# Kernel tuning notes

Measured on AMD Instinct MI355X. Metric: run time of the kernel, lower is better.

The kernel has to match this reference:

```python
import jax, jax.numpy as jnp
import numpy as np

NUM_HEADS = 32
NUM_KV_HEADS = 8
HEAD_DIM = 128


def setup_inputs() -> dict:
    key = jax.random.key(0)
    ks = jax.random.split(key, 5)
    B, S, H = 2, 2048, 4096
    Dq = NUM_HEADS * HEAD_DIM      # 4096
    Dkv = NUM_KV_HEADS * HEAD_DIM  # 1024
    return {
        "hidden_states": jax.random.normal(ks[0], (B, S, H), jnp.float32),
        "w_q": jax.random.normal(ks[1], (H, Dq), jnp.float32) * 0.02,
        "w_k": jax.random.normal(ks[2], (H, Dkv), jnp.float32) * 0.02,
        "w_v": jax.random.normal(ks[3], (H, Dkv), jnp.float32) * 0.02,
        "w_o": jax.random.normal(ks[4], (Dq, H), jnp.float32) * 0.02,
    }


def reference(hidden_states, w_q, w_k, w_v, w_o):
    # GQA causal attention, prefill path (no KV cache, RoPE is a no-op in source).
    B, S, _ = hidden_states.shape
    Hq, Hkv, D = NUM_HEADS, NUM_KV_HEADS, HEAD_DIM
    g = Hq // Hkv  # kv groups
    scale = D ** -0.5

    q = (hidden_states @ w_q).reshape(B, S, Hkv, g, D)  # [B,S,Hkv,g,D]
    k = (hidden_states @ w_k).reshape(B, S, Hkv, D)     # [B,S,Hkv,D]
    v = (hidden_states @ w_v).reshape(B, S, Hkv, D)

    # repeat_kv expressed as grouped einsum (avoids materializing repeated K/V)
    scores = jnp.einsum('bqhgd,bkhd->bhgqk', q, k) * scale  # [B,Hkv,g,S,S]
    causal = jnp.tril(jnp.ones((S, S), dtype=bool))
    scores = jnp.where(causal, scores, -jnp.inf)
    probs = jax.nn.softmax(scores.astype(jnp.float32), axis=-1).astype(q.dtype)

    attn = jnp.einsum('bhgqk,bkhd->bqhgd', probs, v)  # [B,S,Hkv,g,D]
    attn = attn.reshape(B, S, Hq * D)
    return attn @ w_o
```

## Files before the change

kernel.cpp:

```cpp
#include <hip/hip_runtime.h>

typedef unsigned short u16;
typedef __attribute__((ext_vector_type(8))) short bf16x8;
typedef __attribute__((ext_vector_type(8))) unsigned short u16x8;
typedef __attribute__((ext_vector_type(4))) unsigned short u16x4;
typedef __attribute__((ext_vector_type(4))) float f32x4;

__device__ __forceinline__ u16 f2bf(float f) {
  union { float f; unsigned u; } v; v.f = f;
  unsigned r = v.u + 0x7fffu + ((v.u >> 16) & 1u);
  return (u16)(r >> 16);
}

__device__ __forceinline__ void gload16(const u16* g, u16* l) {
  __builtin_amdgcn_global_load_lds((const __attribute__((address_space(1))) void*)g,
                                   (__attribute__((address_space(3))) void*)l, 16, 0, 0);
}

__global__ __launch_bounds__(256) void cast_bf16_kern(const float* __restrict__ in,
                                                      u16* __restrict__ out, int n) {
  int i = (blockIdx.x * 256 + threadIdx.x) * 8;
  if (i >= n) return;
  float4 a = *(const float4*)(in + i);
  float4 b = *(const float4*)(in + i + 4);
  u16x8 r;
  r[0] = f2bf(a.x); r[1] = f2bf(a.y); r[2] = f2bf(a.z); r[3] = f2bf(a.w);
  r[4] = f2bf(b.x); r[5] = f2bf(b.y); r[6] = f2bf(b.z); r[7] = f2bf(b.w);
  *(u16x8*)(out + i) = r;
}

__global__ __launch_bounds__(256) void transpose_cast_kern(const float* __restrict__ in,
                                                           u16* __restrict__ out, int K, int N) {
  __shared__ float tile[64][65];
  int nbx = N >> 6;
  int n0 = (blockIdx.x % nbx) << 6;
  int k0 = (blockIdx.x / nbx) << 6;
  int tx = threadIdx.x & 15;
  int ty = threadIdx.x >> 4;
#pragma unroll
  for (int r = 0; r < 64; r += 16) {
    float4 v = *(const float4*)(in + (size_t)(k0 + ty + r) * N + n0 + tx * 4);
    tile[ty + r][tx * 4 + 0] = v.x;
    tile[ty + r][tx * 4 + 1] = v.y;
    tile[ty + r][tx * 4 + 2] = v.z;
    tile[ty + r][tx * 4 + 3] = v.w;
  }
  __syncthreads();
#pragma unroll
  for (int r = 0; r < 64; r += 16) {
    u16x4 o;
#pragma unroll
    for (int j = 0; j < 4; j++) o[j] = f2bf(tile[tx * 4 + j][ty + r]);
    *(u16x4*)(out + (size_t)(n0 + ty + r) * K + k0 + tx * 4) = o;
  }
}

#define FENCE() asm volatile("" ::: "memory")
#define BARRIER() do { FENCE(); __builtin_amdgcn_s_barrier(); FENCE(); } while (0)

template <int MODE>
__global__ __launch_bounds__(256, 2) void gemm256(const u16* __restrict__ A,
                                                  const u16* __restrict__ Bt,
                                                  void* __restrict__ Cout,
                                                  int M, int N, int K) {
  __shared__ u16 lds[24576];
  const int tid = threadIdx.x;
  const int lane = tid & 63, w = tid >> 6;
  const int wm = w >> 1, wn = w & 1;
  const int li = lane & 15, lg = lane >> 4;
  const int NT = K >> 5;

  const int nbn = N >> 7;
  const int nwg = gridDim.x;
  const int swz = (blockIdx.x & 7) * (nwg >> 3) + (blockIdx.x >> 3);
  const int m0 = (swz / nbn) << 8;
  const int n0 = (swz % nbn) << 7;

  const int ssl = ((lane & 3) ^ ((lane >> 3) & 3)) * 8;
  const u16* sA = A + (size_t)(m0 + w * 64 + (lane >> 2)) * K + ssl;
  const u16* sB = Bt + (size_t)(n0 + w * 32 + (lane >> 2)) * K + ssl;
  const size_t i16K = (size_t)16 * K;
  u16* dA = lds + w * 2048;
  u16* dB = lds + 16384 + w * 1024;

#define STGA(t_) do { int db_ = (t_) & 1;                                    \
    _Pragma("unroll")                                                        \
    for (int i_ = 0; i_ < 4; i_++)                                           \
      gload16(sA + (size_t)(t_) * 32 + i_ * i16K, dA + db_ * 8192 + i_ * 512); \
  } while (0)
#define STGB(t_) do { int db_ = (t_) & 1;                                    \
    _Pragma("unroll")                                                        \
    for (int j_ = 0; j_ < 2; j_++)                                           \
      gload16(sB + (size_t)(t_) * 32 + j_ * i16K, dB + db_ * 4096 + j_ * 512); \
  } while (0)

  STGA(0); STGB(0); STGB(1);
  asm volatile("s_waitcnt vmcnt(2)" ::: "memory");
  BARRIER();

  f32x4 acc[8][4];
#pragma unroll
  for (int m = 0; m < 8; m++)
#pragma unroll
    for (int n = 0; n < 4; n++) acc[m][n] = (f32x4){0.f, 0.f, 0.f, 0.f};

  const int xsl = (lg ^ ((li >> 1) & 3)) * 8;
  const int aoff = (wm * 128 + li) * 32 + xsl;
  const int boff = 16384 + (wn * 64 + li) * 32 + xsl;

  bf16x8 a[8], b[4];

  for (int t = 0; t < NT; ++t) {
    const int db = t & 1;
    const int ao = db * 8192 + aoff;
    const int bo = db * 4096 + boff;

#pragma unroll
    for (int mf = 0; mf < 4; mf++) a[mf] = *(const bf16x8*)(lds + ao + mf * 512);
#pragma unroll
    for (int nf = 0; nf < 4; nf++) b[nf] = *(const bf16x8*)(lds + bo + nf * 512);
    if (t + 1 < NT) STGA(t + 1);
    __builtin_amdgcn_s_setprio(1);
#pragma unroll
    for (int mf = 0; mf < 4; mf++)
#pragma unroll
      for (int nf = 0; nf < 4; nf++)
        acc[mf][nf] = __builtin_amdgcn_mfma_f32_16x16x32_bf16(a[mf], b[nf], acc[mf][nf], 0, 0, 0);
    __builtin_amdgcn_s_setprio(0);
    BARRIER();

#pragma unroll
    for (int mf = 4; mf < 8; mf++) a[mf] = *(const bf16x8*)(lds + ao + mf * 512);
    if (t + 2 < NT) STGB(t + 2);
    __builtin_amdgcn_s_setprio(1);
#pragma unroll
    for (int mf = 4; mf < 8; mf++)
#pragma unroll
      for (int nf = 0; nf < 4; nf++)
        acc[mf][nf] = __builtin_amdgcn_mfma_f32_16x16x32_bf16(a[mf], b[nf], acc[mf][nf], 0, 0, 0);
    __builtin_amdgcn_s_setprio(0);
    if (t < NT - 2) {
      asm volatile("s_waitcnt vmcnt(2)" ::: "memory");
    } else {
      asm volatile("s_waitcnt vmcnt(0)" ::: "memory");
    }
    BARRIER();
  }

#pragma unroll
  for (int mf = 0; mf < 8; mf++)
#pragma unroll
    for (int nf = 0; nf < 4; nf++)
#pragma unroll
      for (int r = 0; r < 4; r++) {
        int gm = m0 + wm * 128 + mf * 16 + lg * 4 + r;
        int gn = n0 + wn * 64 + nf * 16 + li;
        if (MODE == 0)
          ((u16*)Cout)[(size_t)gm * N + gn] = f2bf(acc[mf][nf][r]);
        else
          ((float*)Cout)[(size_t)gm * N + gn] = acc[mf][nf][r];
      }
#undef STGA
#undef STGB
}

__global__ __launch_bounds__(512, 2) void gemm_kv(const u16* __restrict__ A,
                                                  const u16* __restrict__ Bt,
                                                  u16* __restrict__ Kout,
                                                  u16* __restrict__ Vout) {
  __shared__ u16 lds[49152];
  const int tid = threadIdx.x;
  const int lane = tid & 63, w = tid >> 6;
  const int wm = w >> 2, wn = w & 3;
  const int li = lane & 15, lg = lane >> 4;
  const int K = 4096, NT = 64;

  const int swz = (blockIdx.x & 7) * 32 + (blockIdx.x >> 3);
  const int m0 = (swz >> 3) << 7;
  const int n0 = (swz & 7) << 8;

  const int srow = w * 16 + (lane >> 3);
  const int scol = ((lane & 7) ^ (lane >> 3)) << 3;
  const u16* sA  = A  + (size_t)(m0 + srow) * K + scol;
  const u16* sB0 = Bt + (size_t)(n0 + srow) * K + scol;
  const u16* sB1 = Bt + (size_t)(n0 + 128 + srow) * K + scol;
  const size_t jK = (size_t)8 * K;
  u16* dA  = lds + w * 1024;
  u16* dB0 = lds + 16384 + w * 1024;
  u16* dB1 = lds + 16384 + 8192 + w * 1024;

#define STGA(t_) do { int db_ = (t_) & 1;                                     \
    gload16(sA + (size_t)(t_) * 64, dA + db_ * 8192);                         \
    gload16(sA + (size_t)(t_) * 64 + jK, dA + db_ * 8192 + 512); } while (0)
#define STGB(t_) do { int db_ = (t_) & 1;                                     \
    gload16(sB0 + (size_t)(t_) * 64, dB0 + db_ * 16384);                      \
    gload16(sB0 + (size_t)(t_) * 64 + jK, dB0 + db_ * 16384 + 512);           \
    gload16(sB1 + (size_t)(t_) * 64, dB1 + db_ * 16384);                      \
    gload16(sB1 + (size_t)(t_) * 64 + jK, dB1 + db_ * 16384 + 512); } while (0)

  STGA(0); STGB(0); STGB(1);
  asm volatile("s_waitcnt vmcnt(4)" ::: "memory");
  __builtin_amdgcn_s_barrier();
  asm volatile("" ::: "memory");

  f32x4 acc[4][4];
#pragma unroll
  for (int m = 0; m < 4; m++)
#pragma unroll
    for (int n = 0; n < 4; n++) acc[m][n] = (f32x4){0.f, 0.f, 0.f, 0.f};

  const int xsw = (li & 7) << 3;
  const int k0o = (lg * 8) ^ xsw;
  const int k1o = (32 + lg * 8) ^ xsw;
  const int arow0 = wm * 64;
  const u16* bBase0 = lds + 16384 + (wn >> 1) * 8192;
  const int brow0 = (wn & 1) * 64;

  bf16x8 a[4][2], b[4][2];

  for (int t = 0; t < NT; ++t) {
    const int db = t & 1;
    const u16* Ab = lds + db * 8192;
    const u16* Bb = bBase0 + db * 16384;

#pragma unroll
    for (int mf = 0; mf < 2; mf++) {
      int r = arow0 + mf * 16 + li;
      a[mf][0] = *(const bf16x8*)(Ab + r * 64 + k0o);
      a[mf][1] = *(const bf16x8*)(Ab + r * 64 + k1o);
    }
#pragma unroll
    for (int nf = 0; nf < 4; nf++) {
      int r = brow0 + nf * 16 + li;
      b[nf][0] = *(const bf16x8*)(Bb + r * 64 + k0o);
      b[nf][1] = *(const bf16x8*)(Bb + r * 64 + k1o);
    }
    if (t + 1 < NT) STGA(t + 1);
    BARRIER();
    __builtin_amdgcn_s_setprio(1);
#pragma unroll
    for (int mf = 0; mf < 2; mf++)
#pragma unroll
      for (int nf = 0; nf < 4; nf++) {
        acc[mf][nf] = __builtin_amdgcn_mfma_f32_16x16x32_bf16(a[mf][0], b[nf][0], acc[mf][nf], 0, 0, 0);
        acc[mf][nf] = __builtin_amdgcn_mfma_f32_16x16x32_bf16(a[mf][1], b[nf][1], acc[mf][nf], 0, 0, 0);
      }
    __builtin_amdgcn_s_setprio(0);
    BARRIER();

#pragma unroll
    for (int mf = 2; mf < 4; mf++) {
      int r = arow0 + mf * 16 + li;
      a[mf][0] = *(const bf16x8*)(Ab + r * 64 + k0o);
      a[mf][1] = *(const bf16x8*)(Ab + r * 64 + k1o);
    }
    if (t + 2 < NT) STGB(t + 2);
    BARRIER();
    __builtin_amdgcn_s_setprio(1);
#pragma unroll
    for (int mf = 2; mf < 4; mf++)
#pragma unroll
      for (int nf = 0; nf < 4; nf++) {
        acc[mf][nf] = __builtin_amdgcn_mfma_f32_16x16x32_bf16(a[mf][0], b[nf][0], acc[mf][nf], 0, 0, 0);
        acc[mf][nf] = __builtin_amdgcn_mfma_f32_16x16x32_bf16(a[mf][1], b[nf][1], acc[mf][nf], 0, 0, 0);
      }
    __builtin_amdgcn_s_setprio(0);
    if (t < NT - 2) {
      asm volatile("s_waitcnt vmcnt(4)" ::: "memory");
    } else {
      asm volatile("s_waitcnt vmcnt(0)" ::: "memory");
    }
    __builtin_amdgcn_s_barrier();
    asm volatile("" ::: "memory");
  }

#pragma unroll
  for (int mf = 0; mf < 4; mf++)
#pragma unroll
    for (int nf = 0; nf < 4; nf++)
#pragma unroll
      for (int r = 0; r < 4; r++) {
        int gm = m0 + wm * 64 + mf * 16 + lg * 4 + r;
        int gn = n0 + wn * 64 + nf * 16 + li;
        float val = acc[mf][nf][r];
        if (gn < 1024) {
          Kout[(size_t)gm * 1024 + gn] = f2bf(val);
        } else {
          int c = gn - 1024;
          int b = gm >> 11, s = gm & 2047, kvh = c >> 7, d = c & 127;
          int s2 = (s & ~31) | (((s >> 2) & 3) << 3) | (((s >> 4) & 1) << 2) | (s & 3);
          Vout[(size_t)((b * 8 + kvh) * 128 + d) * 2048 + s2] = f2bf(val);
        }
      }
#undef STGA
#undef STGB
}

__global__ __launch_bounds__(256, 2) void flash_attn_kern(const u16* __restrict__ Qg,
                                                          const u16* __restrict__ Kg,
                                                          const u16* __restrict__ VT,
                                                          u16* __restrict__ Og) {
  const int bid = blockIdx.x;
  const int qt = 63 - (bid >> 4);
  const int gh = bid & 15;
  const int b = gh >> 3, kvh = gh & 7;
  const int tid = threadIdx.x;
  const int lane = tid & 63, w = tid >> 6;
  const int li = lane & 15, lg = lane >> 4;
  const int h = kvh * 4 + w;
  const int q0 = qt << 5;
  const int nt = (qt >> 1) + 1;

  __shared__ u16 Kbuf[2][8192];
  __shared__ u16 Vbuf[2][8192];

  bf16x8 qf[2][4];
  {
    const u16* qp = Qg + ((size_t)(b * 2048 + q0 + li)) * 4096 + h * 128 + lg * 8;
#pragma unroll
    for (int m = 0; m < 2; m++)
#pragma unroll
      for (int ks = 0; ks < 4; ks++)
        qf[m][ks] = *(const bf16x8*)(qp + (size_t)(m * 16) * 4096 + ks * 32);
  }

  const u16* ksrc[4];
  const u16* vsrc[4];
#pragma unroll
  for (int i = 0; i < 4; i++) {
    int c = w * 4 + i;
    int krow = c * 4 + (lane >> 4);
    int kinner = ((lane & 15) * 16) ^ ((krow & 7) << 4);
    ksrc[i] = Kg + (size_t)(b * 2048 + krow) * 1024 + kvh * 128 + (kinner >> 1);
    int vrow = c * 8 + (lane >> 3);
    int vinner = ((lane & 7) * 16) ^ ((vrow & 7) << 4);
    vsrc[i] = VT + (size_t)((b * 8 + kvh) * 128 + vrow) * 2048 + (vinner >> 1);
  }
#pragma unroll
  for (int i = 0; i < 4; i++) {
    int c = w * 4 + i;
    gload16(ksrc[i], &Kbuf[0][c * 512]);
    gload16(vsrc[i], &Vbuf[0][c * 512]);
    ksrc[i] += 64 * 1024;
    vsrc[i] += 64;
  }

  f32x4 oa[2][8];
#pragma unroll
  for (int m = 0; m < 2; m++)
#pragma unroll
    for (int n = 0; n < 8; n++) oa[m][n] = (f32x4){0.f, 0.f, 0.f, 0.f};
  f32x4 lacc[2];
  lacc[0] = (f32x4){0.f, 0.f, 0.f, 0.f};
  lacc[1] = (f32x4){0.f, 0.f, 0.f, 0.f};
  float mrun[2] = {-1e30f, -1e30f};

  const float scale = 0.08838834764831845f;
  bf16x8 onesf;
#pragma unroll
  for (int j = 0; j < 8; j++) onesf[j] = (short)0x3F80;

  asm volatile("s_waitcnt vmcnt(0)\n\ts_barrier" ::: "memory");

  for (int t = 0; t < nt; ++t) {
    const int cur = t & 1;
    const u16* KB = Kbuf[cur];
    const u16* VB = Vbuf[cur];
    if (t + 1 < nt) {
#pragma unroll
      for (int i = 0; i < 4; i++) {
        int c = w * 4 + i;
        gload16(ksrc[i], &Kbuf[cur ^ 1][c * 512]);
        gload16(vsrc[i], &Vbuf[cur ^ 1][c * 512]);
        ksrc[i] += 64 * 1024;
        vsrc[i] += 64;
      }
    }

    f32x4 sacc[2][4];
#pragma unroll
    for (int m = 0; m < 2; m++)
#pragma unroll
      for (int n = 0; n < 4; n++) sacc[m][n] = (f32x4){0.f, 0.f, 0.f, 0.f};
    __builtin_amdgcn_s_setprio(1);
#pragma unroll
    for (int n = 0; n < 4; n++) {
      int krow = n * 16 + li;
      const u16* kb = KB + krow * 128;
      int sw = (krow & 7) << 4;
#pragma unroll
      for (int ks = 0; ks < 4; ks++) {
        bf16x8 kf = *(const bf16x8*)(kb + (((ks * 64 + lg * 16) ^ sw) >> 1));
        sacc[0][n] = __builtin_amdgcn_mfma_f32_16x16x32_bf16(kf, qf[0][ks], sacc[0][n], 0, 0, 0);
        sacc[1][n] = __builtin_amdgcn_mfma_f32_16x16x32_bf16(kf, qf[1][ks], sacc[1][n], 0, 0, 0);
      }
    }
    __builtin_amdgcn_s_setprio(0);

#pragma unroll
    for (int m = 0; m < 2; m++)
#pragma unroll
      for (int n = 0; n < 4; n++)
#pragma unroll
        for (int r = 0; r < 4; r++) sacc[m][n][r] *= scale;
    if (t == nt - 1) {
      const int kv0 = t * 64;
#pragma unroll
      for (int m = 0; m < 2; m++) {
        int q = q0 + m * 16 + li;
#pragma unroll
        for (int n = 0; n < 4; n++)
#pragma unroll
          for (int r = 0; r < 4; r++)
            if (kv0 + n * 16 + lg * 4 + r > q) sacc[m][n][r] = -1e30f;
      }
    }

#pragma unroll
    for (int m = 0; m < 2; m++) {
      float mx = sacc[m][0][0];
#pragma unroll
      for (int n = 0; n < 4; n++)
#pragma unroll
        for (int r = 0; r < 4; r++) mx = fmaxf(mx, sacc[m][n][r]);
      mx = fmaxf(mx, __shfl_xor(mx, 16, 64));
      mx = fmaxf(mx, __shfl_xor(mx, 32, 64));
      float mnew = fmaxf(mrun[m], mx);
      float corr = __expf(mrun[m] - mnew);
      mrun[m] = mnew;
#pragma unroll
      for (int n = 0; n < 4; n++)
#pragma unroll
        for (int r = 0; r < 4; r++) sacc[m][n][r] = __expf(sacc[m][n][r] - mnew);
#pragma unroll
      for (int r = 0; r < 4; r++) lacc[m][r] *= corr;
#pragma unroll
      for (int n = 0; n < 8; n++)
#pragma unroll
        for (int r = 0; r < 4; r++) oa[m][n][r] *= corr;
    }

    bf16x8 pf[2][2];
#pragma unroll
    for (int m = 0; m < 2; m++)
#pragma unroll
      for (int kvs = 0; kvs < 2; kvs++) {
        u16x8 pw;
#pragma unroll
        for (int e = 0; e < 8; e++) pw[e] = f2bf(sacc[m][2 * kvs + (e >> 2)][e & 3]);
        pf[m][kvs] = *(bf16x8*)&pw;
      }

    __builtin_amdgcn_s_setprio(1);
#pragma unroll
    for (int kvs = 0; kvs < 2; kvs++) {
#pragma unroll
      for (int n = 0; n < 8; n++) {
        int vrow = n * 16 + li;
        bf16x8 vf = *(const bf16x8*)(VB + vrow * 64 +
                                     (((kvs * 64 + lg * 16) ^ ((vrow & 7) << 4)) >> 1));
        oa[0][n] = __builtin_amdgcn_mfma_f32_16x16x32_bf16(vf, pf[0][kvs], oa[0][n], 0, 0, 0);
        oa[1][n] = __builtin_amdgcn_mfma_f32_16x16x32_bf16(vf, pf[1][kvs], oa[1][n], 0, 0, 0);
      }
      lacc[0] = __builtin_amdgcn_mfma_f32_16x16x32_bf16(onesf, pf[0][kvs], lacc[0], 0, 0, 0);
      lacc[1] = __builtin_amdgcn_mfma_f32_16x16x32_bf16(onesf, pf[1][kvs], lacc[1], 0, 0, 0);
    }
    __builtin_amdgcn_s_setprio(0);

    asm volatile("s_waitcnt vmcnt(0)\n\ts_barrier" ::: "memory");
  }

#pragma unroll
  for (int m = 0; m < 2; m++) {
    float inv = 1.0f / lacc[m][0];
    u16* op = Og + (size_t)(b * 2048 + q0 + m * 16 + li) * 4096 + h * 128 + lg * 4;
#pragma unroll
    for (int n = 0; n < 8; n++) {
      u16x4 o;
#pragma unroll
      for (int r = 0; r < 4; r++) o[r] = f2bf(oa[m][n][r] * inv);
      *(u16x4*)(op + n * 16) = o;
    }
  }
}

extern "C" void kernel_launch(void* const* d_in, const int* in_sizes, int n_in,
                              void* d_out, int out_size, void* d_ws, size_t ws_size,
                              hipStream_t stream) {
  (void)in_sizes; (void)n_in; (void)out_size; (void)ws_size;
  const float* hs = (const float*)d_in[0];
  const float* wq = (const float*)d_in[1];
  const float* wk = (const float*)d_in[2];
  const float* wv = (const float*)d_in[3];
  const float* wo = (const float*)d_in[4];

  u16* ws   = (u16*)d_ws;
  u16* hs_b = ws;
  u16* wqT  = hs_b + 16777216;
  u16* wkT  = wqT + 16777216;
  u16* wvT  = wkT + 4194304;
  u16* woT  = wvT + 4194304;
  u16* Qb   = woT + 16777216;
  u16* Kb   = Qb + 16777216;
  u16* VTb  = Kb + 4194304;
  u16* attnb = VTb + 4194304;

  cast_bf16_kern<<<8192, 256, 0, stream>>>(hs, hs_b, 16777216);
  transpose_cast_kern<<<4096, 256, 0, stream>>>(wq, wqT, 4096, 4096);
  transpose_cast_kern<<<1024, 256, 0, stream>>>(wk, wkT, 4096, 1024);
  transpose_cast_kern<<<1024, 256, 0, stream>>>(wv, wvT, 4096, 1024);
  transpose_cast_kern<<<4096, 256, 0, stream>>>(wo, woT, 4096, 4096);

  gemm256<0><<<512, 256, 0, stream>>>(hs_b, wqT, Qb, 4096, 4096, 4096);
  gemm_kv<<<256, 512, 0, stream>>>(hs_b, wkT, Kb, VTb);

  flash_attn_kern<<<1024, 256, 0, stream>>>(Qb, Kb, VTb, attnb);

  gemm256<2><<<512, 256, 0, stream>>>(attnb, woT, (float*)d_out, 4096, 4096, 4096);
}
```

Baseline: 500.7 us.

## Rewrite Q/O projection GEMM as 256x256 tile with 8-wave ping-pong pipeline

The Q and output projection GEMM moves to a 256x256 block tile with 512 threads and a 64-wide k-step. It uses four-way split A/B LDS buffers, explicit ds_read_b128 inline asm with immediate offsets, and lgkmcnt-controlled interleaving of global-to-LDS prefetch with MFMA quarters. The aim is to raise arithmetic intensity per LDS and global byte and to overlap loads with compute more finely. The 128KB LDS footprint limits occupancy to one block per CU, and the grid shrinks to 256 blocks.

```diff
diff --git a/kernel.cpp b/kernel.cpp
--- a/kernel.cpp
+++ b/kernel.cpp
@@ -16,6 +16,19 @@
   __builtin_amdgcn_global_load_lds((const __attribute__((address_space(1))) void*)g,
                                    (__attribute__((address_space(3))) void*)l, 16, 0, 0);
 }
+
+template <int OFF>
+__device__ __forceinline__ bf16x8 dsr(unsigned a) {
+  static_assert(OFF >= 0 && OFF < 65536, "ds offset");
+  bf16x8 r;
+  asm volatile("ds_read_b128 %0, %1 offset:%2" : "=&v"(r) : "v"(a), "n"(OFF));
+  return r;
+}
+
+#define FENCE() asm volatile("" ::: "memory")
+#define BARRIER() do { FENCE(); __builtin_amdgcn_s_barrier(); FENCE(); } while (0)
+#define LGKM(n) do { asm volatile("s_waitcnt lgkmcnt(" #n ")" ::: "memory"); \
+                     __builtin_amdgcn_sched_barrier(0); } while (0)
 
 __global__ __launch_bounds__(256) void cast_bf16_kern(const float* __restrict__ in,
                                                       u16* __restrict__ out, int n) {
@@ -55,47 +68,49 @@
   }
 }
 
-#define FENCE() asm volatile("" ::: "memory")
-#define BARRIER() do { FENCE(); __builtin_amdgcn_s_barrier(); FENCE(); } while (0)
-
 template <int MODE>
-__global__ __launch_bounds__(256, 2) void gemm256(const u16* __restrict__ A,
+__global__ __launch_bounds__(512, 2) void gemm256(const u16* __restrict__ A,
                                                   const u16* __restrict__ Bt,
                                                   void* __restrict__ Cout,
                                                   int M, int N, int K) {
-  __shared__ u16 lds[24576];
+  __shared__ u16 lds[65536];
   const int tid = threadIdx.x;
   const int lane = tid & 63, w = tid >> 6;
-  const int wm = w >> 1, wn = w & 1;
+  const int wm = w >> 2, wn = w & 3;
   const int li = lane & 15, lg = lane >> 4;
-  const int NT = K >> 5;
-
-  const int nbn = N >> 7;
+  const int NT = K >> 6, NU = NT >> 1;
+
+  const int nbx = N >> 8;
   const int nwg = gridDim.x;
   const int swz = (blockIdx.x & 7) * (nwg >> 3) + (blockIdx.x >> 3);
-  const int m0 = (swz / nbn) << 8;
-  const int n0 = (swz % nbn) << 7;
-
-  const int ssl = ((lane & 3) ^ ((lane >> 3) & 3)) * 8;
-  const u16* sA = A + (size_t)(m0 + w * 64 + (lane >> 2)) * K + ssl;
-  const u16* sB = Bt + (size_t)(n0 + w * 32 + (lane >> 2)) * K + ssl;
-  const size_t i16K = (size_t)16 * K;
-  u16* dA = lds + w * 2048;
-  u16* dB = lds + 16384 + w * 1024;
-
-#define STGA(t_) do { int db_ = (t_) & 1;                                    \
-    _Pragma("unroll")                                                        \
-    for (int i_ = 0; i_ < 4; i_++)                                           \
-      gload16(sA + (size_t)(t_) * 32 + i_ * i16K, dA + db_ * 8192 + i_ * 512); \
+  const int m0 = (swz / nbx) << 8;
+  const int n0 = (swz % nbx) << 8;
+
+  const int srow = w * 16 + (lane >> 3);
+  const int scol = ((lane & 7) ^ (lane >> 3)) << 3;
+  const u16* sA0 = A + (size_t)(m0 + srow) * K + scol;
+  const u16* sA1 = A + (size_t)(m0 + 128 + srow) * K + scol;
+  const u16* sB0 = Bt + (size_t)(n0 + srow) * K + scol;
+  const u16* sB1 = Bt + (size_t)(n0 + 128 + srow) * K + scol;
+  const size_t jK = (size_t)8 * K;
+  u16* const dEA0 = lds + w * 1024;
+  u16* const dEA1 = lds + 8192 + w * 1024;
+  u16* const dOA0 = lds + 16384 + w * 1024;
+  u16* const dOA1 = lds + 24576 + w * 1024;
+  u16* const dEB0 = lds + 32768 + w * 1024;
+  u16* const dEB1 = lds + 40960 + w * 1024;
+  u16* const dOB0 = lds + 49152 + w * 1024;
+  u16* const dOB1 = lds + 57344 + w * 1024;
+
+#define STGH(sp, dp, t_) do {                                   \
+    gload16((sp) + (size_t)(t_) * 64, (dp));                    \
+    gload16((sp) + (size_t)(t_) * 64 + jK, (dp) + 512);         \
   } while (0)
-#define STGB(t_) do { int db_ = (t_) & 1;                                    \
-    _Pragma("unroll")                                                        \
-    for (int j_ = 0; j_ < 2; j_++)                                           \
-      gload16(sB + (size_t)(t_) * 32 + j_ * i16K, dB + db_ * 4096 + j_ * 512); \
-  } while (0)
-
-  STGA(0); STGB(0); STGB(1);
-  asm volatile("s_waitcnt vmcnt(2)" ::: "memory");
+
+  STGH(sA0, dEA0, 0); STGH(sA1, dEA1, 0);
+  STGH(sB0, dEB0, 0); STGH(sB1, dEB1, 0);
+  STGH(sA0, dOA0, 1); STGH(sA1, dOA1, 1);
+  asm volatile("s_waitcnt vmcnt(4)" ::: "memory");
   BARRIER();
 
   f32x4 acc[8][4];
@@ -104,46 +119,97 @@
 #pragma unroll
     for (int n = 0; n < 4; n++) acc[m][n] = (f32x4){0.f, 0.f, 0.f, 0.f};
 
-  const int xsl = (lg ^ ((li >> 1) & 3)) * 8;
-  const int aoff = (wm * 128 + li) * 32 + xsl;
-  const int boff = 16384 + (wn * 64 + li) * 32 + xsl;
-
-  bf16x8 a[8], b[4];
-
-  for (int t = 0; t < NT; ++t) {
-    const int db = t & 1;
-    const int ao = db * 8192 + aoff;
-    const int bo = db * 4096 + boff;
-
-#pragma unroll
-    for (int mf = 0; mf < 4; mf++) a[mf] = *(const bf16x8*)(lds + ao + mf * 512);
-#pragma unroll
-    for (int nf = 0; nf < 4; nf++) b[nf] = *(const bf16x8*)(lds + bo + nf * 512);
-    if (t + 1 < NT) STGA(t + 1);
-    __builtin_amdgcn_s_setprio(1);
-#pragma unroll
-    for (int mf = 0; mf < 4; mf++)
-#pragma unroll
-      for (int nf = 0; nf < 4; nf++)
-        acc[mf][nf] = __builtin_amdgcn_mfma_f32_16x16x32_bf16(a[mf], b[nf], acc[mf][nf], 0, 0, 0);
-    __builtin_amdgcn_s_setprio(0);
-    BARRIER();
-
-#pragma unroll
-    for (int mf = 4; mf < 8; mf++) a[mf] = *(const bf16x8*)(lds + ao + mf * 512);
-    if (t + 2 < NT) STGB(t + 2);
-    __builtin_amdgcn_s_setprio(1);
-#pragma unroll
-    for (int mf = 4; mf < 8; mf++)
-#pragma unroll
-      for (int nf = 0; nf < 4; nf++)
-        acc[mf][nf] = __builtin_amdgcn_mfma_f32_16x16x32_bf16(a[mf], b[nf], acc[mf][nf], 0, 0, 0);
-    __builtin_amdgcn_s_setprio(0);
-    if (t < NT - 2) {
-      asm volatile("s_waitcnt vmcnt(2)" ::: "memory");
-    } else {
-      asm volatile("s_waitcnt vmcnt(0)" ::: "memory");
-    }
+  const int xb = ((li & 7) << 3);
+  const unsigned lbase = (unsigned)(size_t)(&lds[0]);
+  const unsigned adA0 = lbase + (unsigned)(wm * 16384 + li * 128 + (((lg * 8) ^ xb) << 1));
+  const unsigned adA1 = lbase + (unsigned)(wm * 16384 + li * 128 + ((((32 + lg * 8)) ^ xb) << 1));
+  const unsigned adB0 = lbase + 65536u +
+      (unsigned)((wn >> 1) * 16384 + ((wn & 1) * 64 + li) * 128 + (((lg * 8) ^ xb) << 1));
+  const unsigned adB1 = lbase + 65536u +
+      (unsigned)((wn >> 1) * 16384 + ((wn & 1) * 64 + li) * 128 + ((((32 + lg * 8)) ^ xb) << 1));
+
+  bf16x8 al[4][2], ah[4][2], b[4][2];
+
+#define MFMA1 __builtin_amdgcn_mfma_f32_16x16x32_bf16
+#define Q_MFMA(ACCB, AF, NF0)                                               \
+  __builtin_amdgcn_s_setprio(1);                                            \
+  _Pragma("unroll")                                                         \
+  for (int ks = 0; ks < 2; ks++)                                            \
+    _Pragma("unroll")                                                       \
+    for (int mf = 0; mf < 4; mf++)                                          \
+      _Pragma("unroll")                                                     \
+      for (int nf = NF0; nf < NF0 + 2; nf++)                                \
+        acc[ACCB + mf][nf] = MFMA1(AF[mf][ks], b[nf][ks], acc[ACCB + mf][nf], 0, 0, 0); \
+  __builtin_amdgcn_s_setprio(0)
+
+  for (int u = 0; u < NU; ++u) {
+    const int tE = 2 * u, tO = 2 * u + 1;
+    const bool pf = (u + 1 < NU);
+
+    STGH(sB0, dOB0, tO);
+    al[0][0] = dsr<0>(adA0);     al[1][0] = dsr<2048>(adA0);
+    al[2][0] = dsr<4096>(adA0);  al[3][0] = dsr<6144>(adA0);
+    al[0][1] = dsr<0>(adA1);     al[1][1] = dsr<2048>(adA1);
+    al[2][1] = dsr<4096>(adA1);  al[3][1] = dsr<6144>(adA1);
+    b[0][0] = dsr<0>(adB0);      b[1][0] = dsr<2048>(adB0);
+    b[0][1] = dsr<0>(adB1);      b[1][1] = dsr<2048>(adB1);
+    b[2][0] = dsr<4096>(adB0);   b[3][0] = dsr<6144>(adB0);
+    b[2][1] = dsr<4096>(adB1);   b[3][1] = dsr<6144>(adB1);
+    LGKM(4);
+    Q_MFMA(0, al, 0);
+    BARRIER();
+
+    STGH(sB1, dOB1, tO);
+    ah[0][0] = dsr<8192>(adA0);   ah[1][0] = dsr<10240>(adA0);
+    ah[2][0] = dsr<12288>(adA0);  ah[3][0] = dsr<14336>(adA0);
+    ah[0][1] = dsr<8192>(adA1);   ah[1][1] = dsr<10240>(adA1);
+    ah[2][1] = dsr<12288>(adA1);  ah[3][1] = dsr<14336>(adA1);
+    LGKM(8);
+    Q_MFMA(0, al, 2);
+    BARRIER();
+
+    if (pf) STGH(sA0, dEA0, tE + 2);
+    LGKM(0);
+    Q_MFMA(4, ah, 2);
+    BARRIER();
+
+    if (pf) STGH(sA1, dEA1, tE + 2);
+    Q_MFMA(4, ah, 0);
+    if (pf) { asm volatile("s_waitcnt vmcnt(4)" ::: "memory"); }
+    else    { asm volatile("s_waitcnt vmcnt(0)" ::: "memory"); }
+    BARRIER();
+
+    if (pf) STGH(sB0, dEB0, tE + 2);
+    al[0][0] = dsr<32768>(adA0);  al[1][0] = dsr<34816>(adA0);
+    al[2][0] = dsr<36864>(adA0);  al[3][0] = dsr<38912>(adA0);
+    al[0][1] = dsr<32768>(adA1);  al[1][1] = dsr<34816>(adA1);
+    al[2][1] = dsr<36864>(adA1);  al[3][1] = dsr<38912>(adA1);
+    b[0][0] = dsr<32768>(adB0);   b[1][0] = dsr<34816>(adB0);
+    b[0][1] = dsr<32768>(adB1);   b[1][1] = dsr<34816>(adB1);
+    b[2][0] = dsr<36864>(adB0);   b[3][0] = dsr<38912>(adB0);
+    b[2][1] = dsr<36864>(adB1);   b[3][1] = dsr<38912>(adB1);
+    LGKM(4);
+    Q_MFMA(0, al, 0);
+    BARRIER();
+
+    if (pf) STGH(sB1, dEB1, tE + 2);
+    ah[0][0] = dsr<40960>(adA0);  ah[1][0] = dsr<43008>(adA0);
+    ah[2][0] = dsr<45056>(adA0);  ah[3][0] = dsr<47104>(adA0);
+    ah[0][1] = dsr<40960>(adA1);  ah[1][1] = dsr<43008>(adA1);
+    ah[2][1] = dsr<45056>(adA1);  ah[3][1] = dsr<47104>(adA1);
+    LGKM(8);
+    Q_MFMA(0, al, 2);
+    BARRIER();
+
+    if (pf) STGH(sA0, dOA0, tO + 2);
+    LGKM(0);
+    Q_MFMA(4, ah, 2);
+    BARRIER();
+
+    if (pf) STGH(sA1, dOA1, tO + 2);
+    Q_MFMA(4, ah, 0);
+    if (pf) { asm volatile("s_waitcnt vmcnt(4)" ::: "memory"); }
+    else    { asm volatile("s_waitcnt vmcnt(0)" ::: "memory"); }
     BARRIER();
   }
 
@@ -160,8 +226,9 @@
         else
           ((float*)Cout)[(size_t)gm * N + gn] = acc[mf][nf][r];
       }
-#undef STGA
-#undef STGB
+#undef STGH
+#undef Q_MFMA
+#undef MFMA1
 }
 
 __global__ __launch_bounds__(512, 2) void gemm_kv(const u16* __restrict__ A,
@@ -511,10 +578,10 @@
   transpose_cast_kern<<<1024, 256, 0, stream>>>(wv, wvT, 4096, 1024);
   transpose_cast_kern<<<4096, 256, 0, stream>>>(wo, woT, 4096, 4096);
 
-  gemm256<0><<<512, 256, 0, stream>>>(hs_b, wqT, Qb, 4096, 4096, 4096);
+  gemm256<0><<<256, 512, 0, stream>>>(hs_b, wqT, Qb, 4096, 4096, 4096);
   gemm_kv<<<256, 512, 0, stream>>>(hs_b, wkT, Kb, VTb);
 
   flash_attn_kern<<<1024, 256, 0, stream>>>(Qb, Kb, VTb, attnb);
 
-  gemm256<2><<<512, 256, 0, stream>>>(attnb, woT, (float*)d_out, 4096, 4096, 4096);
-}
+  gemm256<2><<<256, 512, 0, stream>>>(attnb, woT, (float*)d_out, 4096, 4096, 4096);
+}
```

After: 553.6 us. 10.6% more time.
